# Performance work log

Hardware: AMD Instinct MI355X
Metric: run time of the kernel (lower is better)

The kernel has to match this reference:

```python
import jax, jax.numpy as jnp
import numpy as np

B, N, DEG = 256, 16384, 32  # batch, num_neurons, fan-in per neuron

def setup_inputs() -> dict:
    key = jax.random.key(0)
    kx, kw, ki = jax.random.split(key, 3)
    x = jax.random.normal(kx, (B, N), dtype=jnp.float32)
    w = jax.random.normal(kw, (N, DEG), dtype=jnp.float32)  # nonzero weights per neuron
    idx = jax.random.randint(ki, (N, DEG), 0, N)            # source-neuron indices per neuron
    return {"x": x, "w": w, "idx": idx}

def reference(x, w, idx):
    # Per neuron j: gather its fan-in channels and apply Dense(1) with
    # kernel = nonzero weights, then relu; concat over neurons == axis N.
    gathered = x[:, idx]                      # [B, N, DEG] gather
    out = jnp.einsum('bnd,nd->bn', gathered, w)  # sparse matvec per batch row
    return jax.nn.relu(out)                   # [B, N]
```

## Files before the change

kernel.cpp:

```cpp
#include <hip/hip_runtime.h>


#define B      256
#define N      16384
#define DEG    32
#define NT     32
#define NCHUNK 4
#define CB     64

typedef float v4f __attribute__((ext_vector_type(4)));
typedef _Float16 h8v __attribute__((ext_vector_type(8)));

__global__ __launch_bounds__(256) void chunk_transpose_f16_kernel(
    const float* __restrict__ x, _Float16* __restrict__ xc) {
    __shared__ float tile[64][65];
    const int t     = threadIdx.x;
    const int j0    = blockIdx.x * 64;
    const int chunk = blockIdx.y;
    const int c4 = t & 15;
    const int r  = t >> 4;

#pragma unroll
    for (int it = 0; it < 4; ++it) {
        const int row = r + it * 16;
        const float4 v = *(const float4*)&x[(size_t)(chunk * 64 + row) * N + j0 + 4 * c4];
        tile[row][4 * c4 + 0] = v.x;
        tile[row][4 * c4 + 1] = v.y;
        tile[row][4 * c4 + 2] = v.z;
        tile[row][4 * c4 + 3] = v.w;
    }
    __syncthreads();

    const int wv = t >> 6, l = t & 63;
    const int a  = l & 7;
    _Float16* dst = xc + (size_t)chunk * N * CB + 8 * a;
#pragma unroll
    for (int p = 0; p < 2; ++p) {
        const int j = p * 32 + wv * 8 + (l >> 3);
        h8v h;
#pragma unroll
        for (int k = 0; k < 8; ++k) h[k] = (_Float16)tile[8 * a + k][j];
        *(h8v*)&dst[(size_t)(j0 + j) * CB] = h;
    }
}

__global__ __launch_bounds__(256, 8) void gather_dot_f16_kernel(
    const _Float16* __restrict__ xc, const float* __restrict__ w,
    const int* __restrict__ idx, float* __restrict__ out) {
    __shared__ __align__(16) float smem[64 * 33];
    int*   sidx = (int*)smem;
    float* sw   = smem + 1024;

    const int t     = threadIdx.x;
    const int chunk = blockIdx.x & 3;
    const int nb    = (int)(blockIdx.x >> 2) * NT;
    const int wv    = t >> 6;
    const int l     = t & 63;
    const int slot  = wv * 8 + (l >> 3);
    const int a     = l & 7;

    {
        const int n_l = t >> 3, d4 = t & 7;
        ((int4*)sidx)[d4 * 32 + n_l] = ((const int4*)(idx + (size_t)nb * DEG))[t];
        ((float4*)sw)[d4 * 32 + n_l] = ((const float4*)(w + (size_t)nb * DEG))[t];
    }
    __syncthreads();

    const _Float16* xcb = xc + (size_t)chunk * N * CB + 8 * a;

    float acc[8] = {0.f, 0.f, 0.f, 0.f, 0.f, 0.f, 0.f, 0.f};
#pragma unroll
    for (int d4 = 0; d4 < DEG / 4; ++d4) {
        const int4   j4 = ((const int4*)sidx)[d4 * 32 + slot];
        const float4 w4 = ((const float4*)sw)[d4 * 32 + slot];
        const h8v v0 = *(const h8v*)&xcb[(size_t)j4.x * CB];
        const h8v v1 = *(const h8v*)&xcb[(size_t)j4.y * CB];
        const h8v v2 = *(const h8v*)&xcb[(size_t)j4.z * CB];
        const h8v v3 = *(const h8v*)&xcb[(size_t)j4.w * CB];
#pragma unroll
        for (int k = 0; k < 8; ++k) acc[k] = fmaf(w4.x, (float)v0[k], acc[k]);
#pragma unroll
        for (int k = 0; k < 8; ++k) acc[k] = fmaf(w4.y, (float)v1[k], acc[k]);
#pragma unroll
        for (int k = 0; k < 8; ++k) acc[k] = fmaf(w4.z, (float)v2[k], acc[k]);
#pragma unroll
        for (int k = 0; k < 8; ++k) acc[k] = fmaf(w4.w, (float)v3[k], acc[k]);
    }
    __syncthreads();

    float* tile = smem;
#pragma unroll
    for (int k = 0; k < 8; ++k)
        tile[(8 * a + k) * 33 + slot] = acc[k];
    __syncthreads();

#pragma unroll
    for (int p = 0; p < 2; ++p) {
        const int b = wv * 16 + p * 8 + (l >> 3);
        const int c = l & 7;
        v4f v;
        v.x = fmaxf(tile[b * 33 + 4 * c + 0], 0.f);
        v.y = fmaxf(tile[b * 33 + 4 * c + 1], 0.f);
        v.z = fmaxf(tile[b * 33 + 4 * c + 2], 0.f);
        v.w = fmaxf(tile[b * 33 + 4 * c + 3], 0.f);
        __builtin_nontemporal_store(v, (v4f*)&out[(size_t)(chunk * CB + b) * N + nb + 4 * c]);
    }
}

extern "C" void kernel_launch(void* const* d_in, const int* in_sizes, int n_in,
                              void* d_out, int out_size, void* d_ws, size_t ws_size,
                              hipStream_t stream) {
    const float* x   = (const float*)d_in[0];
    const float* w   = (const float*)d_in[1];
    const int*   idx = (const int*)d_in[2];
    float* out = (float*)d_out;
    _Float16* xc = (_Float16*)d_ws;

    dim3 tgrid(N / 64, B / 64);
    chunk_transpose_f16_kernel<<<tgrid, 256, 0, stream>>>(x, xc);

    gather_dot_f16_kernel<<<(N / NT) * NCHUNK, 256, 0, stream>>>(xc, w, idx, out);
}
```

Measured before the change: 90.86 us.

## Load idx/w directly into registers and software-pipeline gathers in gather_dot

The gather kernel no longer stages idx and w through shared memory behind a barrier. Each thread now loads its neuron's 32 indices and weights straight into registers, and the gathers are software-pipelined with four register buffers so 16 gathers are in flight while earlier ones are consumed. The occupancy hint in launch_bounds is dropped and the output store is no longer nontemporal. This removes the prologue barrier and raises memory-level parallelism, but it needs many more registers, which may lower occupancy. The 8 lanes of a slot each issue the same redundant idx/w loads.

```diff
diff --git a/kernel.cpp b/kernel.cpp
--- a/kernel.cpp
+++ b/kernel.cpp
@@ -44,12 +44,10 @@
     }
 }
 
-__global__ __launch_bounds__(256, 8) void gather_dot_f16_kernel(
+__global__ __launch_bounds__(256) void gather_dot_f16_kernel(
     const _Float16* __restrict__ xc, const float* __restrict__ w,
     const int* __restrict__ idx, float* __restrict__ out) {
-    __shared__ __align__(16) float smem[64 * 33];
-    int*   sidx = (int*)smem;
-    float* sw   = smem + 1024;
+    __shared__ float tile[64 * 33];
 
     const int t     = threadIdx.x;
     const int chunk = blockIdx.x & 3;
@@ -58,37 +56,58 @@
     const int l     = t & 63;
     const int slot  = wv * 8 + (l >> 3);
     const int a     = l & 7;
+    const int n     = nb + slot;
 
-    {
-        const int n_l = t >> 3, d4 = t & 7;
-        ((int4*)sidx)[d4 * 32 + n_l] = ((const int4*)(idx + (size_t)nb * DEG))[t];
-        ((float4*)sw)[d4 * 32 + n_l] = ((const float4*)(w + (size_t)nb * DEG))[t];
-    }
-    __syncthreads();
+    const int4*   idx4 = (const int4*)(idx + (size_t)n * DEG);
+    const float4* w4p  = (const float4*)(w   + (size_t)n * DEG);
+    int4 j[8];
+#pragma unroll
+    for (int d4 = 0; d4 < 8; ++d4) j[d4] = idx4[d4];
+    float4 wq[8];
+#pragma unroll
+    for (int d4 = 0; d4 < 8; ++d4) wq[d4] = w4p[d4];
 
-    const _Float16* xcb = xc + (size_t)chunk * N * CB + 8 * a;
+    const _Float16* xcb = xc + (size_t)chunk * (N * CB) + 8 * a;
+
+#define GATHER(g, jv)                                   \
+    g[0] = *(const h8v*)&xcb[(size_t)(jv).x * CB];      \
+    g[1] = *(const h8v*)&xcb[(size_t)(jv).y * CB];      \
+    g[2] = *(const h8v*)&xcb[(size_t)(jv).z * CB];      \
+    g[3] = *(const h8v*)&xcb[(size_t)(jv).w * CB];
 
     float acc[8] = {0.f, 0.f, 0.f, 0.f, 0.f, 0.f, 0.f, 0.f};
-#pragma unroll
-    for (int d4 = 0; d4 < DEG / 4; ++d4) {
-        const int4   j4 = ((const int4*)sidx)[d4 * 32 + slot];
-        const float4 w4 = ((const float4*)sw)[d4 * 32 + slot];
-        const h8v v0 = *(const h8v*)&xcb[(size_t)j4.x * CB];
-        const h8v v1 = *(const h8v*)&xcb[(size_t)j4.y * CB];
-        const h8v v2 = *(const h8v*)&xcb[(size_t)j4.z * CB];
-        const h8v v3 = *(const h8v*)&xcb[(size_t)j4.w * CB];
-#pragma unroll
-        for (int k = 0; k < 8; ++k) acc[k] = fmaf(w4.x, (float)v0[k], acc[k]);
-#pragma unroll
-        for (int k = 0; k < 8; ++k) acc[k] = fmaf(w4.y, (float)v1[k], acc[k]);
-#pragma unroll
-        for (int k = 0; k < 8; ++k) acc[k] = fmaf(w4.z, (float)v2[k], acc[k]);
-#pragma unroll
-        for (int k = 0; k < 8; ++k) acc[k] = fmaf(w4.w, (float)v3[k], acc[k]);
+
+#define CONSUME(g, W)                                                     \
+    {                                                                     \
+        _Pragma("unroll")                                                 \
+        for (int k = 0; k < 8; ++k) acc[k] = fmaf((W).x, (float)g[0][k], acc[k]); \
+        _Pragma("unroll")                                                 \
+        for (int k = 0; k < 8; ++k) acc[k] = fmaf((W).y, (float)g[1][k], acc[k]); \
+        _Pragma("unroll")                                                 \
+        for (int k = 0; k < 8; ++k) acc[k] = fmaf((W).z, (float)g[2][k], acc[k]); \
+        _Pragma("unroll")                                                 \
+        for (int k = 0; k < 8; ++k) acc[k] = fmaf((W).w, (float)g[3][k], acc[k]); \
     }
+
+    h8v g0[4], g1[4], g2[4], g3[4];
+    GATHER(g0, j[0]);
+    GATHER(g1, j[1]);
+    GATHER(g2, j[2]);
+    GATHER(g3, j[3]);
+
+    CONSUME(g0, wq[0]); GATHER(g0, j[4]);
+    CONSUME(g1, wq[1]); GATHER(g1, j[5]);
+    CONSUME(g2, wq[2]); GATHER(g2, j[6]);
+    CONSUME(g3, wq[3]); GATHER(g3, j[7]);
+    CONSUME(g0, wq[4]);
+    CONSUME(g1, wq[5]);
+    CONSUME(g2, wq[6]);
+    CONSUME(g3, wq[7]);
+
+#undef GATHER
+#undef CONSUME
+
     __syncthreads();
-
-    float* tile = smem;
 #pragma unroll
     for (int k = 0; k < 8; ++k)
         tile[(8 * a + k) * 33 + slot] = acc[k];
@@ -103,7 +122,7 @@
         v.y = fmaxf(tile[b * 33 + 4 * c + 1], 0.f);
         v.z = fmaxf(tile[b * 33 + 4 * c + 2], 0.f);
         v.w = fmaxf(tile[b * 33 + 4 * c + 3], 0.f);
-        __builtin_nontemporal_store(v, (v4f*)&out[(size_t)(chunk * CB + b) * N + nb + 4 * c]);
+        *(v4f*)&out[(size_t)(chunk * CB + b) * N + nb + 4 * c] = v;
     }
 }
 
```

Result: slower. 92.76 us (+2.1%).
